# Kernel tuning notes

Hardware: AMD Instinct MI355X
Metric: run time of the kernel (lower is better)

The kernel has to match this reference:

```python
import jax, jax.numpy as jnp
import numpy as np

N = 50000
E = 800000
F_IN, F_HID, F_OUT = 128, 64, 40


def setup_inputs() -> dict:
    key = jax.random.key(0)
    ks = jax.random.split(key, 8)
    x = jax.random.normal(ks[0], (N, F_IN), dtype=jnp.float32)
    edge_index = jax.random.randint(ks[1], (2, E), 0, N, dtype=jnp.int64)
    # Glorot-style init like PyG GCNConv.lin; stored as [in, out]
    def glorot(k, fi, fo):
        s = jnp.sqrt(6.0 / (fi + fo)).astype(jnp.float32)
        return jax.random.uniform(k, (fi, fo), jnp.float32, -s, s)
    W1 = glorot(ks[2], F_IN, F_HID)
    b1 = jnp.zeros((F_HID,), jnp.float32)
    W2 = glorot(ks[3], F_HID, F_HID)
    b2 = jnp.zeros((F_HID,), jnp.float32)
    W3 = glorot(ks[4], F_HID, F_OUT)
    b3 = jnp.zeros((F_OUT,), jnp.float32)
    return {"x": x, "edge_index": edge_index, "W1": W1, "b1": b1,
            "W2": W2, "b2": b2, "W3": W3, "b3": b3}


def _prep_edges(edge_index):
    # add self-loops, compute symmetric GCN normalization (as PyG gcn_norm)
    loops = jnp.arange(N, dtype=edge_index.dtype)
    src = jnp.concatenate([edge_index[0], loops])
    dst = jnp.concatenate([edge_index[1], loops])
    deg = jax.ops.segment_sum(jnp.ones_like(dst, dtype=jnp.float32), dst,
                              num_segments=N)
    dinv = jnp.where(deg > 0, jax.lax.rsqrt(deg), 0.0)
    norm = dinv[src] * dinv[dst]  # [E+N]
    return src, dst, norm


def _gcn_conv(x, W, b, src, dst, norm):
    h = x @ W                                  # [N, out] dense projection
    msg = h[src] * norm[:, None]               # gather + scale, [E+N, out]
    out = jax.ops.segment_sum(msg, dst, num_segments=N)  # scatter-add
    return out + b


def reference(x, edge_index, W1, b1, W2, b2, W3, b3):
    src, dst, norm = _prep_edges(edge_index)
    h = jax.nn.relu(_gcn_conv(x, W1, b1, src, dst, norm))
    h = jax.nn.relu(_gcn_conv(h, W2, b2, src, dst, norm))
    return _gcn_conv(h, W3, b3, src, dst, norm)
```

## Files before the change

### kernel.cpp

```cpp
#include <hip/hip_runtime.h>
#include <hip/hip_fp16.h>
#include <math.h>

#define NN 50000
#define EE 800000
#define FIN 128
#define FHID 64
#define FOUT 40

#define BSH  6
#define NBKT ((NN + 63) >> 6)
#define CAP  1600
#define KBBLK 128
#define CHK  (EE / KBBLK)


__global__ void k_detect(const unsigned int* __restrict__ w, int* __restrict__ flag,
                         int* __restrict__ gcur) {
    int t = threadIdx.x;
    if (t < NBKT) gcur[t] = t * CAP;
    if (t == 0) *flag = 1;
    __syncthreads();
    unsigned v = w[2 * t + 1];
    unsigned long long b = __ballot(v != 0);
    if (b && (t & 63) == 0) atomicAnd(flag, 0);
}


__global__ __launch_bounds__(256) void k_bucket(const unsigned int* __restrict__ w,
                                                const int* __restrict__ flag,
                                                int* __restrict__ gcur,
                                                unsigned int* __restrict__ BKT) {
    __shared__ int hist[NBKT], rsv[NBKT], lcur[NBKT];
    const int tid = threadIdx.x;
    for (int i = tid; i < NBKT; i += 256) { hist[i] = 0; lcur[i] = 0; }
    __syncthreads();
    const bool f64 = (*flag) != 0;
    const int e0 = blockIdx.x * CHK, e1 = e0 + CHK;

    for (int e = e0 + tid; e < e1; e += 256) {
        unsigned d = f64 ? w[2 * (EE + e)] : w[EE + e];
        atomicAdd(&hist[d >> BSH], 1);
    }
    __syncthreads();
    for (int i = tid; i < NBKT; i += 256) {
        int h = hist[i];
        rsv[i] = h ? atomicAdd(&gcur[i], h) : 0;
    }
    __syncthreads();
    for (int e = e0 + tid; e < e1; e += 256) {
        unsigned s, d;
        if (f64) { s = w[2 * e]; d = w[2 * (EE + e)]; }
        else     { s = w[e];     d = w[EE + e]; }
        unsigned b = d >> BSH;
        int idx = atomicAdd(&lcur[b], 1);
        BKT[rsv[b] + idx] = (d << 16) | s;
    }
}

__global__ __launch_bounds__(256) void k_bscan(const int* __restrict__ gcur,
                                               int* __restrict__ base) {
    __shared__ int ws[4];
    __shared__ int carry;
    const int tid  = threadIdx.x;
    const int lane = tid & 63;
    const int wid  = tid >> 6;
    if (tid == 0) carry = 0;
    __syncthreads();
    for (int b0 = 0; b0 < NBKT; b0 += 256) {
        int i = b0 + tid;
        int v = (i < NBKT) ? (gcur[i] - i * CAP) : 0;
        int incl = v;
#pragma unroll
        for (int o = 1; o < 64; o <<= 1) {
            int u = __shfl_up(incl, o, 64);
            if (lane >= o) incl += u;
        }
        if (lane == 63) ws[wid] = incl;
        __syncthreads();
        int c = carry;
        int wofs = 0;
#pragma unroll
        for (int q = 0; q < 4; q++) if (q < wid) wofs += ws[q];
        if (i < NBKT) base[i] = c + wofs + incl - v;
        __syncthreads();
        if (tid == 0) carry = c + ws[0] + ws[1] + ws[2] + ws[3];
    }
    if (tid == 0) base[NBKT] = carry;
}

__global__ __launch_bounds__(256) void k_fine(const unsigned int* __restrict__ BKT,
                                              const int* __restrict__ gcur,
                                              const int* __restrict__ base,
                                              int* __restrict__ off,
                                              float* __restrict__ dinv,
                                              unsigned short* __restrict__ ebuf) {
    __shared__ unsigned st[CAP];
    __shared__ int h[64], sc[64], lc[64];
    const int tid = threadIdx.x;
    const int b   = blockIdx.x;
    int cnt = gcur[b] - b * CAP;
    if (cnt > CAP) cnt = CAP;
    const int bb = base[b];
    if (tid < 64) { h[tid] = 0; lc[tid] = 0; }
    __syncthreads();
    for (int i = tid; i < cnt; i += 256) {
        unsigned p = BKT[b * CAP + i];
        st[i] = p;
        atomicAdd(&h[(p >> 16) & 63], 1);
    }
    __syncthreads();
    if (tid < 64) {
        int v = h[tid];
        int incl = v;
#pragma unroll
        for (int o = 1; o < 64; o <<= 1) {
            int u = __shfl_up(incl, o, 64);
            if (tid >= o) incl += u;
        }
        sc[tid] = incl - v;
        int n = (b << BSH) + tid;
        if (n < NN) {
            off[n]  = bb + sc[tid];
            dinv[n] = 1.0f / sqrtf((float)(v + 1));
        }
    }
    if (b == 0 && tid == 64) off[NN] = EE;
    __syncthreads();
    for (int i = tid; i < cnt; i += 256) {
        unsigned p = st[i];
        int l = (p >> 16) & 63;
        int idx = atomicAdd(&lc[l], 1);
        ebuf[bb + sc[l] + idx] = (unsigned short)(p & 0xffffu);
    }
}


template <int K, int MREAL, bool XF16>
__global__ __launch_bounds__(256) void k_gemm_h(const void* __restrict__ Xv,
                                                const float* __restrict__ W,
                                                const float* __restrict__ dinv,
                                                unsigned short* __restrict__ Ph) {
    constexpr int ROWS = 16;
    constexpr int XP = K + 4;
    __shared__ float Ws[K * 64];
    __shared__ float Xs[ROWS * XP];
    const int tid  = threadIdx.x;
    const int row0 = blockIdx.x * ROWS;
    const int row_end = (NN - row0 < ROWS) ? (NN - row0) : ROWS;

    if constexpr (MREAL == 64) {
        for (int i = tid; i < K * 16; i += 256)
            ((float4*)Ws)[i] = ((const float4*)W)[i];
    } else {
        for (int i = tid; i < K * 64; i += 256) {
            int col = i & 63, row = i >> 6;
            Ws[i] = (col < MREAL) ? W[row * MREAL + col] : 0.f;
        }
    }
    for (int i = tid; i < row_end * (K / 4); i += 256) {
        int r = i / (K / 4), c = i % (K / 4);
        if constexpr (XF16) {
            uint2 u = ((const uint2*)Xv)[(size_t)(row0 + r) * (K / 4) + c];
            __half2 h01 = *reinterpret_cast<const __half2*>(&u.x);
            __half2 h23 = *reinterpret_cast<const __half2*>(&u.y);
            Xs[r * XP + 4 * c + 0] = __low2float(h01);
            Xs[r * XP + 4 * c + 1] = __high2float(h01);
            Xs[r * XP + 4 * c + 2] = __low2float(h23);
            Xs[r * XP + 4 * c + 3] = __high2float(h23);
        } else {
            float4 v = ((const float4*)Xv)[(size_t)(row0 + r) * (K / 4) + c];
            *(float4*)&Xs[r * XP + 4 * c] = v;
        }
    }
    __syncthreads();

    const int r  = tid >> 4;
    const int cg = tid & 15;
    const int grow = row0 + r;
    if (r >= row_end) return;

    float a0 = 0.f, a1 = 0.f, a2 = 0.f, a3 = 0.f;
#pragma unroll 4
    for (int k = 0; k < K; k++) {
        float xv = Xs[r * XP + k];
        float4 wv = *(const float4*)&Ws[k * 64 + cg * 4];
        a0 = fmaf(xv, wv.x, a0);
        a1 = fmaf(xv, wv.y, a1);
        a2 = fmaf(xv, wv.z, a2);
        a3 = fmaf(xv, wv.w, a3);
    }
    float dv = dinv[grow];
    ushort4 o;
    o.x = __half_as_ushort(__float2half_rn(a0 * dv));
    o.y = __half_as_ushort(__float2half_rn(a1 * dv));
    o.z = __half_as_ushort(__float2half_rn(a2 * dv));
    o.w = __half_as_ushort(__float2half_rn(a3 * dv));
    *(ushort4*)&Ph[(size_t)grow * 64 + cg * 4] = o;
}


__device__ __forceinline__ void acc_h(float4& acc, uint2 u) {
    __half2 h01 = *reinterpret_cast<const __half2*>(&u.x);
    __half2 h23 = *reinterpret_cast<const __half2*>(&u.y);
    acc.x += __low2float(h01);
    acc.y += __high2float(h01);
    acc.z += __low2float(h23);
    acc.w += __high2float(h23);
}

template <int OUTQ, bool RELU, bool OUTF16>
__global__ __launch_bounds__(256) void k_agg4h(const uint2* __restrict__ Pu,
                                               const int* __restrict__ off,
                                               const unsigned short* __restrict__ ebuf,
                                               const float* __restrict__ dinv,
                                               const float4* __restrict__ bias4,
                                               void* __restrict__ outv) {
    const int gid  = blockIdx.x * blockDim.x + threadIdx.x;
    const int node = gid >> 6;
    const int lane = threadIdx.x & 63;
    if (node >= NN) return;
    const int g = lane >> 4;
    const int q = lane & 15;
    const int s = off[node];
    const int e = off[node + 1];

    float4 acc = {0.f, 0.f, 0.f, 0.f};
    if (g == 0) acc_h(acc, Pu[(size_t)node * 16 + q]);

    int i = s;
    for (; i + 15 < e; i += 16) {
        int c0 = ebuf[i + g], c1 = ebuf[i + g + 4], c2 = ebuf[i + g + 8], c3 = ebuf[i + g + 12];
        uint2 u0 = Pu[(size_t)c0 * 16 + q];
        uint2 u1 = Pu[(size_t)c1 * 16 + q];
        uint2 u2 = Pu[(size_t)c2 * 16 + q];
        uint2 u3 = Pu[(size_t)c3 * 16 + q];
        acc_h(acc, u0); acc_h(acc, u1); acc_h(acc, u2); acc_h(acc, u3);
    }
    if (i < e) {
        int j0 = i + g, j1 = i + g + 4, j2 = i + g + 8, j3 = i + g + 12;
        uint2 u0 = Pu[(size_t)ebuf[j0 < e ? j0 : e - 1] * 16 + q];
        uint2 u1 = Pu[(size_t)ebuf[j1 < e ? j1 : e - 1] * 16 + q];
        uint2 u2 = Pu[(size_t)ebuf[j2 < e ? j2 : e - 1] * 16 + q];
        uint2 u3 = Pu[(size_t)ebuf[j3 < e ? j3 : e - 1] * 16 + q];
        if (j0 < e) acc_h(acc, u0);
        if (j1 < e) acc_h(acc, u1);
        if (j2 < e) acc_h(acc, u2);
        if (j3 < e) acc_h(acc, u3);
    }

#pragma unroll
    for (int o = 16; o <= 32; o <<= 1) {
        acc.x += __shfl_xor(acc.x, o, 64);
        acc.y += __shfl_xor(acc.y, o, 64);
        acc.z += __shfl_xor(acc.z, o, 64);
        acc.w += __shfl_xor(acc.w, o, 64);
    }

    if (lane < OUTQ) {
        float dv = dinv[node];
        float4 b = bias4[q];
        float4 v;
        v.x = fmaf(acc.x, dv, b.x);
        v.y = fmaf(acc.y, dv, b.y);
        v.z = fmaf(acc.z, dv, b.z);
        v.w = fmaf(acc.w, dv, b.w);
        if (RELU) {
            v.x = fmaxf(v.x, 0.f); v.y = fmaxf(v.y, 0.f);
            v.z = fmaxf(v.z, 0.f); v.w = fmaxf(v.w, 0.f);
        }
        if constexpr (OUTF16) {
            ushort4 o;
            o.x = __half_as_ushort(__float2half_rn(v.x));
            o.y = __half_as_ushort(__float2half_rn(v.y));
            o.z = __half_as_ushort(__float2half_rn(v.z));
            o.w = __half_as_ushort(__float2half_rn(v.w));
            ((ushort4*)outv)[(size_t)node * 16 + q] = o;
        } else {
            ((float4*)outv)[(size_t)node * OUTQ + q] = v;
        }
    }
}


static inline size_t alignup(size_t x) { return (x + 255) & ~(size_t)255; }

extern "C" void kernel_launch(void* const* d_in, const int* in_sizes, int n_in,
                              void* d_out, int out_size, void* d_ws, size_t ws_size,
                              hipStream_t stream) {
    const float*        x  = (const float*)d_in[0];
    const unsigned int* ew = (const unsigned int*)d_in[1];
    const float*        W1 = (const float*)d_in[2];
    const float*        b1 = (const float*)d_in[3];
    const float*        W2 = (const float*)d_in[4];
    const float*        b2 = (const float*)d_in[5];
    const float*        W3 = (const float*)d_in[6];
    const float*        b3 = (const float*)d_in[7];

    char* w = (char*)d_ws;
    int*            flag = (int*)w;            w += alignup(4);
    int*            gcur = (int*)w;            w += alignup(NBKT * 4);
    int*            base = (int*)w;            w += alignup((NBKT + 1) * 4);
    int*            off  = (int*)w;            w += alignup((NN + 1) * 4);
    float*          dinv = (float*)w;          w += alignup(NN * 4);
    unsigned int*   BKT  = (unsigned int*)w;   w += alignup((size_t)NBKT * CAP * 4);
    unsigned short* ebuf = (unsigned short*)w; w += alignup(EE * 2);
    unsigned short* Ph   = (unsigned short*)w; w += alignup((size_t)NN * 64 * 2);
    unsigned short* Hh   = (unsigned short*)w; w += alignup((size_t)NN * 64 * 2);

    const int BA = (NN * 64) / 256;
    const int BG = (NN + 15) / 16;

    k_detect<<<1, 1024, 0, stream>>>(ew, flag, gcur);
    k_bucket<<<KBBLK, 256, 0, stream>>>(ew, flag, gcur, BKT);
    k_bscan<<<1, 256, 0, stream>>>(gcur, base);
    k_fine<<<NBKT, 256, 0, stream>>>(BKT, gcur, base, off, dinv, ebuf);

    k_gemm_h<FIN, FHID, false><<<BG, 256, 0, stream>>>(x, W1, dinv, Ph);
    k_agg4h<16, true, true><<<BA, 256, 0, stream>>>((const uint2*)Ph, off, ebuf, dinv,
                                                    (const float4*)b1, Hh);

    k_gemm_h<FHID, FHID, true><<<BG, 256, 0, stream>>>(Hh, W2, dinv, Ph);
    k_agg4h<16, true, true><<<BA, 256, 0, stream>>>((const uint2*)Ph, off, ebuf, dinv,
                                                    (const float4*)b2, Hh);

    k_gemm_h<FHID, FOUT, true><<<BG, 256, 0, stream>>>(Hh, W3, dinv, Ph);
    k_agg4h<10, false, false><<<BA, 256, 0, stream>>>((const uint2*)Ph, off, ebuf, dinv,
                                                      (const float4*)b3, d_out);
}
```

Baseline: 243.7 us.

## Fuse aggregation with next-layer GEMM and drop bucket-scan kernel

Layers 2 and 3 now aggregate first and then apply the weight matrix. This uses (A·H)W = A·(HW): a fused kernel gathers the 64-wide row sum into shared memory and multiplies it by W in the same block, and the separate GEMM kernels and one intermediate round trip go away. The layer-1 aggregation pre-multiplies its output by dinv so the next gather needs no extra scaling. The single-block bucket prefix-scan kernel is removed; each fine-sort block instead recomputes its own base by summing earlier bucket counts, which is redundant O(NBKT) work per block. The fused kernel does a serial 64-long dot product per lane per node, with only 4 nodes per wave, so compute per node may rise.

```diff
diff --git a/kernel.cpp b/kernel.cpp
--- a/kernel.cpp
+++ b/kernel.cpp
@@ -58,52 +58,30 @@
     }
 }
 
-__global__ __launch_bounds__(256) void k_bscan(const int* __restrict__ gcur,
-                                               int* __restrict__ base) {
-    __shared__ int ws[4];
-    __shared__ int carry;
-    const int tid  = threadIdx.x;
-    const int lane = tid & 63;
-    const int wid  = tid >> 6;
-    if (tid == 0) carry = 0;
-    __syncthreads();
-    for (int b0 = 0; b0 < NBKT; b0 += 256) {
-        int i = b0 + tid;
-        int v = (i < NBKT) ? (gcur[i] - i * CAP) : 0;
-        int incl = v;
-#pragma unroll
-        for (int o = 1; o < 64; o <<= 1) {
-            int u = __shfl_up(incl, o, 64);
-            if (lane >= o) incl += u;
-        }
-        if (lane == 63) ws[wid] = incl;
-        __syncthreads();
-        int c = carry;
-        int wofs = 0;
-#pragma unroll
-        for (int q = 0; q < 4; q++) if (q < wid) wofs += ws[q];
-        if (i < NBKT) base[i] = c + wofs + incl - v;
-        __syncthreads();
-        if (tid == 0) carry = c + ws[0] + ws[1] + ws[2] + ws[3];
-    }
-    if (tid == 0) base[NBKT] = carry;
-}
-
 __global__ __launch_bounds__(256) void k_fine(const unsigned int* __restrict__ BKT,
                                               const int* __restrict__ gcur,
-                                              const int* __restrict__ base,
                                               int* __restrict__ off,
                                               float* __restrict__ dinv,
                                               unsigned short* __restrict__ ebuf) {
     __shared__ unsigned st[CAP];
     __shared__ int h[64], sc[64], lc[64];
-    const int tid = threadIdx.x;
-    const int b   = blockIdx.x;
+    __shared__ int red[4];
+    const int tid  = threadIdx.x;
+    const int lane = tid & 63;
+    const int wid  = tid >> 6;
+    const int b    = blockIdx.x;
+
+    int partial = 0;
+    for (int i = tid; i < b; i += 256) partial += gcur[i] - i * CAP;
+#pragma unroll
+    for (int o = 1; o < 64; o <<= 1) partial += __shfl_xor(partial, o, 64);
+    if (lane == 0) red[wid] = partial;
+    if (tid < 64) { h[tid] = 0; lc[tid] = 0; }
+    __syncthreads();
+    const int bb = red[0] + red[1] + red[2] + red[3];
+
     int cnt = gcur[b] - b * CAP;
     if (cnt > CAP) cnt = CAP;
-    const int bb = base[b];
-    if (tid < 64) { h[tid] = 0; lc[tid] = 0; }
-    __syncthreads();
     for (int i = tid; i < cnt; i += 256) {
         unsigned p = BKT[b * CAP + i];
         st[i] = p;
@@ -136,42 +114,23 @@
 }
 
 
-template <int K, int MREAL, bool XF16>
-__global__ __launch_bounds__(256) void k_gemm_h(const void* __restrict__ Xv,
-                                                const float* __restrict__ W,
-                                                const float* __restrict__ dinv,
-                                                unsigned short* __restrict__ Ph) {
-    constexpr int ROWS = 16;
-    constexpr int XP = K + 4;
+__global__ __launch_bounds__(256) void k_gemm1(const float* __restrict__ X,
+                                               const float* __restrict__ W,
+                                               const float* __restrict__ dinv,
+                                               unsigned short* __restrict__ Ph) {
+    constexpr int K = FIN, ROWS = 16, XP = K + 4;
     __shared__ float Ws[K * 64];
     __shared__ float Xs[ROWS * XP];
     const int tid  = threadIdx.x;
     const int row0 = blockIdx.x * ROWS;
     const int row_end = (NN - row0 < ROWS) ? (NN - row0) : ROWS;
 
-    if constexpr (MREAL == 64) {
-        for (int i = tid; i < K * 16; i += 256)
-            ((float4*)Ws)[i] = ((const float4*)W)[i];
-    } else {
-        for (int i = tid; i < K * 64; i += 256) {
-            int col = i & 63, row = i >> 6;
-            Ws[i] = (col < MREAL) ? W[row * MREAL + col] : 0.f;
-        }
-    }
+    for (int i = tid; i < K * 16; i += 256)
+        ((float4*)Ws)[i] = ((const float4*)W)[i];
     for (int i = tid; i < row_end * (K / 4); i += 256) {
         int r = i / (K / 4), c = i % (K / 4);
-        if constexpr (XF16) {
-            uint2 u = ((const uint2*)Xv)[(size_t)(row0 + r) * (K / 4) + c];
-            __half2 h01 = *reinterpret_cast<const __half2*>(&u.x);
-            __half2 h23 = *reinterpret_cast<const __half2*>(&u.y);
-            Xs[r * XP + 4 * c + 0] = __low2float(h01);
-            Xs[r * XP + 4 * c + 1] = __high2float(h01);
-            Xs[r * XP + 4 * c + 2] = __low2float(h23);
-            Xs[r * XP + 4 * c + 3] = __high2float(h23);
-        } else {
-            float4 v = ((const float4*)Xv)[(size_t)(row0 + r) * (K / 4) + c];
-            *(float4*)&Xs[r * XP + 4 * c] = v;
-        }
+        float4 v = ((const float4*)X)[(size_t)(row0 + r) * (K / 4) + c];
+        *(float4*)&Xs[r * XP + 4 * c] = v;
     }
     __syncthreads();
 
@@ -209,25 +168,11 @@
     acc.w += __high2float(h23);
 }
 
-template <int OUTQ, bool RELU, bool OUTF16>
-__global__ __launch_bounds__(256) void k_agg4h(const uint2* __restrict__ Pu,
-                                               const int* __restrict__ off,
-                                               const unsigned short* __restrict__ ebuf,
-                                               const float* __restrict__ dinv,
-                                               const float4* __restrict__ bias4,
-                                               void* __restrict__ outv) {
-    const int gid  = blockIdx.x * blockDim.x + threadIdx.x;
-    const int node = gid >> 6;
-    const int lane = threadIdx.x & 63;
-    if (node >= NN) return;
-    const int g = lane >> 4;
-    const int q = lane & 15;
-    const int s = off[node];
-    const int e = off[node + 1];
-
+__device__ __forceinline__ float4 gather_row_sum(const uint2* __restrict__ Pu,
+                                                 const unsigned short* __restrict__ ebuf,
+                                                 int node, int s, int e, int g, int q) {
     float4 acc = {0.f, 0.f, 0.f, 0.f};
     if (g == 0) acc_h(acc, Pu[(size_t)node * 16 + q]);
-
     int i = s;
     for (; i + 15 < e; i += 16) {
         int c0 = ebuf[i + g], c1 = ebuf[i + g + 4], c2 = ebuf[i + g + 8], c3 = ebuf[i + g + 12];
@@ -248,7 +193,6 @@
         if (j2 < e) acc_h(acc, u2);
         if (j3 < e) acc_h(acc, u3);
     }
-
 #pragma unroll
     for (int o = 16; o <= 32; o <<= 1) {
         acc.x += __shfl_xor(acc.x, o, 64);
@@ -256,28 +200,85 @@
         acc.z += __shfl_xor(acc.z, o, 64);
         acc.w += __shfl_xor(acc.w, o, 64);
     }
-
-    if (lane < OUTQ) {
+    return acc;
+}
+
+
+__global__ __launch_bounds__(256) void k_agg1(const uint2* __restrict__ Pu,
+                                              const int* __restrict__ off,
+                                              const unsigned short* __restrict__ ebuf,
+                                              const float* __restrict__ dinv,
+                                              const float4* __restrict__ bias4,
+                                              unsigned short* __restrict__ HA) {
+    const int gid  = blockIdx.x * blockDim.x + threadIdx.x;
+    const int node = gid >> 6;
+    const int lane = threadIdx.x & 63;
+    if (node >= NN) return;
+    const int g = lane >> 4, q = lane & 15;
+    float4 acc = gather_row_sum(Pu, ebuf, node, off[node], off[node + 1], g, q);
+    if (lane < 16) {
         float dv = dinv[node];
         float4 b = bias4[q];
         float4 v;
-        v.x = fmaf(acc.x, dv, b.x);
-        v.y = fmaf(acc.y, dv, b.y);
-        v.z = fmaf(acc.z, dv, b.z);
-        v.w = fmaf(acc.w, dv, b.w);
-        if (RELU) {
-            v.x = fmaxf(v.x, 0.f); v.y = fmaxf(v.y, 0.f);
-            v.z = fmaxf(v.z, 0.f); v.w = fmaxf(v.w, 0.f);
+        v.x = fmaxf(fmaf(acc.x, dv, b.x), 0.f) * dv;
+        v.y = fmaxf(fmaf(acc.y, dv, b.y), 0.f) * dv;
+        v.z = fmaxf(fmaf(acc.z, dv, b.z), 0.f) * dv;
+        v.w = fmaxf(fmaf(acc.w, dv, b.w), 0.f) * dv;
+        ushort4 o;
+        o.x = __half_as_ushort(__float2half_rn(v.x));
+        o.y = __half_as_ushort(__float2half_rn(v.y));
+        o.z = __half_as_ushort(__float2half_rn(v.z));
+        o.w = __half_as_ushort(__float2half_rn(v.w));
+        ((ushort4*)HA)[(size_t)node * 16 + q] = o;
+    }
+}
+
+
+template <int MOUT, bool OUTF16>
+__global__ __launch_bounds__(256) void k_fuse(const uint2* __restrict__ Hu,
+                                              const float* __restrict__ W,
+                                              const int* __restrict__ off,
+                                              const unsigned short* __restrict__ ebuf,
+                                              const float* __restrict__ dinv,
+                                              const float* __restrict__ bias,
+                                              void* __restrict__ outv) {
+    __shared__ float Ws[64 * MOUT];
+    __shared__ float aggL[4 * 64];
+    const int tid  = threadIdx.x;
+    const int lane = tid & 63;
+    const int wv   = tid >> 6;
+    const int g = lane >> 4, q = lane & 15;
+
+    for (int i = tid; i < 64 * MOUT / 4; i += 256)
+        ((float4*)Ws)[i] = ((const float4*)W)[i];
+    __syncthreads();
+
+    const float bv = (lane < MOUT) ? bias[lane] : 0.f;
+    const int n0 = blockIdx.x * 16 + wv * 4;
+
+#pragma unroll 1
+    for (int j = 0; j < 4; j++) {
+        const int node = n0 + j;
+        float4 acc = gather_row_sum(Hu, ebuf, node, off[node], off[node + 1], g, q);
+        const float dv = dinv[node];
+        if (lane < 16) {
+            float4 t;
+            t.x = acc.x * dv; t.y = acc.y * dv; t.z = acc.z * dv; t.w = acc.w * dv;
+            *(float4*)&aggL[wv * 64 + q * 4] = t;
         }
-        if constexpr (OUTF16) {
-            ushort4 o;
-            o.x = __half_as_ushort(__float2half_rn(v.x));
-            o.y = __half_as_ushort(__float2half_rn(v.y));
-            o.z = __half_as_ushort(__float2half_rn(v.z));
-            o.w = __half_as_ushort(__float2half_rn(v.w));
-            ((ushort4*)outv)[(size_t)node * 16 + q] = o;
-        } else {
-            ((float4*)outv)[(size_t)node * OUTQ + q] = v;
+        if (lane < MOUT) {
+            float o = 0.f;
+#pragma unroll 8
+            for (int k = 0; k < 64; k++)
+                o = fmaf(aggL[wv * 64 + k], Ws[k * MOUT + lane], o);
+            float v = o + bv;
+            if constexpr (OUTF16) {
+                v = fmaxf(v, 0.f);
+                ((unsigned short*)outv)[(size_t)node * 64 + lane] =
+                    __half_as_ushort(__float2half_rn(v * dv));
+            } else {
+                ((float*)outv)[(size_t)node * MOUT + lane] = v;
+            }
         }
     }
 }
@@ -300,31 +301,28 @@
     char* w = (char*)d_ws;
     int*            flag = (int*)w;            w += alignup(4);
     int*            gcur = (int*)w;            w += alignup(NBKT * 4);
-    int*            base = (int*)w;            w += alignup((NBKT + 1) * 4);
     int*            off  = (int*)w;            w += alignup((NN + 1) * 4);
     float*          dinv = (float*)w;          w += alignup(NN * 4);
     unsigned int*   BKT  = (unsigned int*)w;   w += alignup((size_t)NBKT * CAP * 4);
     unsigned short* ebuf = (unsigned short*)w; w += alignup(EE * 2);
     unsigned short* Ph   = (unsigned short*)w; w += alignup((size_t)NN * 64 * 2);
-    unsigned short* Hh   = (unsigned short*)w; w += alignup((size_t)NN * 64 * 2);
+    unsigned short* HA   = (unsigned short*)w; w += alignup((size_t)NN * 64 * 2);
+    unsigned short* HB   = (unsigned short*)w; w += alignup((size_t)NN * 64 * 2);
 
     const int BA = (NN * 64) / 256;
     const int BG = (NN + 15) / 16;
 
     k_detect<<<1, 1024, 0, stream>>>(ew, flag, gcur);
     k_bucket<<<KBBLK, 256, 0, stream>>>(ew, flag, gcur, BKT);
-    k_bscan<<<1, 256, 0, stream>>>(gcur, base);
-    k_fine<<<NBKT, 256, 0, stream>>>(BKT, gcur, base, off, dinv, ebuf);
-
-    k_gemm_h<FIN, FHID, false><<<BG, 256, 0, stream>>>(x, W1, dinv, Ph);
-    k_agg4h<16, true, true><<<BA, 256, 0, stream>>>((const uint2*)Ph, off, ebuf, dinv,
-                                                    (const float4*)b1, Hh);
-
-    k_gemm_h<FHID, FHID, true><<<BG, 256, 0, stream>>>(Hh, W2, dinv, Ph);
-    k_agg4h<16, true, true><<<BA, 256, 0, stream>>>((const uint2*)Ph, off, ebuf, dinv,
-                                                    (const float4*)b2, Hh);
-
-    k_gemm_h<FHID, FOUT, true><<<BG, 256, 0, stream>>>(Hh, W3, dinv, Ph);
-    k_agg4h<10, false, false><<<BA, 256, 0, stream>>>((const uint2*)Ph, off, ebuf, dinv,
-                                                      (const float4*)b3, d_out);
-}
+    k_fine<<<NBKT, 256, 0, stream>>>(BKT, gcur, off, dinv, ebuf);
+
+    k_gemm1<<<BG, 256, 0, stream>>>(x, W1, dinv, Ph);
+    k_agg1<<<BA, 256, 0, stream>>>((const uint2*)Ph, off, ebuf, dinv,
+                                   (const float4*)b1, HA);
+
+    k_fuse<FHID, true><<<BG, 256, 0, stream>>>((const uint2*)HA, W2, off, ebuf,
+                                               dinv, b2, HB);
+
+    k_fuse<FOUT, false><<<BG, 256, 0, stream>>>((const uint2*)HB, W3, off, ebuf,
+                                                dinv, b3, d_out);
+}
```

Result: faster. 220.6 us (-9.5%).
